# Kernel tuning notes

Measured on AMD Instinct MI355X. Metric: run time of the kernel, lower is better.

## Reference

```python
import jax, jax.numpy as jnp
import numpy as np

G = 3            # number of groups
K = 40           # per-group vector dim
CODEBOOK_SIZE = 1024
VQ_COMMIT = 0.25


def setup_inputs() -> dict:
    key = jax.random.key(0)
    k1, k2 = jax.random.split(key)
    z = jax.random.normal(k1, (32, 30, 16384), dtype=jnp.float32)
    codebooks = jax.random.normal(k2, (G, CODEBOOK_SIZE, K), dtype=jnp.float32)
    return {"z": z, "codebooks": codebooks}


def _group_vq(z, codebooks):
    N, C, T = z.shape
    # torch: z = reshape(z, (N, C*4, -1)); assert C*4 == K*G
    z4 = z.reshape(N, C * 4, T // 4)              # (N, G*K, T')
    Tp = z4.shape[2]
    # split channels into G contiguous blocks of K, flatten to vectors of dim K
    x = z4.reshape(N, G, K, Tp).transpose(1, 0, 3, 2).reshape(G, N * Tp, K)  # (G, M, K)
    # squared-L2 nearest-codeword search (cdist + argmin), batched over groups
    x2 = jnp.sum(x * x, axis=-1, keepdims=True)           # (G, M, 1)
    e2 = jnp.sum(codebooks * codebooks, axis=-1)          # (G, S)
    d = x2 + e2[:, None, :] - 2.0 * jnp.einsum('gmk,gsk->gms', x, codebooks)  # (G, M, S)
    idx = jnp.argmin(d, axis=-1)                          # (G, M)
    q = jax.vmap(lambda cb, i: cb[i])(codebooks, idx)     # (G, M, K)
    # torch loop overwrites vq_loss each iteration -> only last group's commitment loss survives
    vq_loss = VQ_COMMIT * jnp.mean((jax.lax.stop_gradient(q[-1]) - x[-1]) ** 2)
    # straight-through estimator
    q_st = x + jax.lax.stop_gradient(q - x)               # (G, M, K)
    # undo the group split/flatten, then reshape back to (N, C, T)
    q_merge = q_st.reshape(G, N, Tp, K).transpose(1, 0, 3, 2).reshape(N, G * K, Tp)
    q_merge = q_merge.reshape(N, C, T)
    return q_merge, vq_loss


def reference(z, codebooks):
    return _group_vq(z, codebooks)
```

## Files before the change

### kernel.cpp

```cpp
#include <hip/hip_runtime.h>

#define G 3
#define K 40
#define S 1024
#define NB 32
#define CH 30
#define T 16384
#define TP 4096
#define M 131072
#define CT (CH*T)
#define OUT_Q (NB*CH*T)
#define MARGIN 4e-3f
#define FLAGBIT 0x40000000u

typedef __attribute__((ext_vector_type(8))) short short8;
typedef __attribute__((ext_vector_type(4))) float f32x4;

#define WS_LOSS 0
#define WS_E2   64
#define WS_PX   12352

static __device__ __forceinline__ unsigned short f2bf(float f) {
    union { float f; unsigned int u; } v; v.f = f;
    unsigned int u = v.u;
    return (unsigned short)((u + 0x7fffu + ((u >> 16) & 1u)) >> 16);
}
static __device__ __forceinline__ float bf2f(unsigned short h) {
    union { unsigned int u; float f; } v; v.u = ((unsigned int)h) << 16;
    return v.f;
}


__global__ void vq_prep_frag(const float* __restrict__ cb, short8* __restrict__ PX,
                             float* __restrict__ e2, double* __restrict__ loss) {
    int t = blockIdx.x * 256 + threadIdx.x;
    if (t == 0) *loss = 0.0;
    if (t >= G * 64 * 64) return;
    const int lane = t & 63;
    const int st   = (t >> 6) & 63;
    const int g    = t >> 12;
    const int lmod = lane & 15, lgrp = lane >> 4;
    const int s0   = st * 16;
    const float* cbg = cb + (size_t)g * S * K;

    if (lane < 16) {
        const float* row = cbg + (size_t)(s0 + lane) * K;
        float acc = 0.f;
        #pragma unroll
        for (int k = 0; k < K; ++k) acc = fmaf(row[k], row[k], acc);
        e2[g * S + s0 + lane] = -0.5f * acc;
    }

    const float* crow = cbg + (size_t)(s0 + lmod) * K;
    #pragma unroll
    for (int m = 0; m < 4; ++m) {
        short8 P;
        #pragma unroll
        for (int j = 0; j < 8; ++j) {
            int kap = 32 * m + 8 * lgrp + j;
            bool valid = kap < 120;
            int d = (kap < 40) ? kap : ((kap < 80) ? kap - 40 : kap - 80);
            float v = valid ? crow[d] : 0.f;
            unsigned short hh = f2bf(v);
            unsigned short ll = f2bf(v - bf2f(hh));
            bool low = (kap >= 40) && (kap < 80);
            P[j] = (short)(low ? ll : hh);
        }
        PX[(((size_t)(g * 64 + st)) * 4 + m) * 64 + lane] = P;
    }
}

__global__ __launch_bounds__(256, 4) void vq_search(
        const float* __restrict__ z, const short8* __restrict__ PX,
        const float* __restrict__ e2, float* __restrict__ out) {
    __shared__ float sE2[S];

    const int lane = threadIdx.x & 63;
    const int w    = threadIdx.x >> 6;
    const int g    = blockIdx.x >> 10;
    const int qbase = ((blockIdx.x & 1023) << 7) + (w << 5);
    const int n    = qbase >> 12;
    const int tp0  = qbase & 4095;
    const int lmod = lane & 15, lgrp = lane >> 4;

    const float* zg  = z + (size_t)n * CT + (size_t)g * K * TP;
    const float* e2g = e2 + g * S;
    const short8* PXg = PX + ((size_t)g * 64) * 4 * 64;

    *(f32x4*)(sE2 + threadIdx.x * 4) = *(const f32x4*)(e2g + threadIdx.x * 4);

    short8 xq[2][4];
    #pragma unroll
    for (int mt = 0; mt < 2; ++mt) {
        int tp = tp0 + mt * 16 + lmod;
        #pragma unroll
        for (int m = 0; m < 4; ++m) {
            short8 xb;
            #pragma unroll
            for (int j = 0; j < 8; ++j) {
                int kap = 32 * m + 8 * lgrp + j;
                bool valid = kap < 120;
                int d = (kap < 40) ? kap : ((kap < 80) ? kap - 40 : kap - 80);
                float v = valid ? zg[(size_t)d * TP + tp] : 0.f;
                unsigned short hh = f2bf(v);
                unsigned short ll = f2bf(v - bf2f(hh));
                bool low = (kap >= 80) && (kap < 120);
                xb[j] = (short)(low ? ll : hh);
            }
            xq[mt][m] = xb;
        }
    }
    __syncthreads();

    float v1[2], v2[2]; int i1[2];
    #pragma unroll
    for (int mt = 0; mt < 2; ++mt) { v1[mt] = -3.4e38f; v2[mt] = -3.4e38f; i1[mt] = 0; }

#define COMPTILE(c0_, c1_, c2_, c3_, st_)                                               \
    do {                                                                                \
        f32x4 e2v = *(const f32x4*)(sE2 + (st_) * 16 + lgrp * 4);                       \
        const int sbase = (st_) * 16 + lgrp * 4;                                        \
        _Pragma("unroll")                                                               \
        for (int mt = 0; mt < 2; ++mt) {                                                \
            f32x4 d = __builtin_amdgcn_mfma_f32_16x16x32_bf16(c0_, xq[mt][0], e2v, 0, 0, 0); \
            d = __builtin_amdgcn_mfma_f32_16x16x32_bf16(c1_, xq[mt][1], d, 0, 0, 0);    \
            d = __builtin_amdgcn_mfma_f32_16x16x32_bf16(c2_, xq[mt][2], d, 0, 0, 0);    \
            d = __builtin_amdgcn_mfma_f32_16x16x32_bf16(c3_, xq[mt][3], d, 0, 0, 0);    \
            _Pragma("unroll")                                                           \
            for (int j = 0; j < 4; ++j) {                                               \
                float sj = d[j];                                                        \
                v2[mt] = __builtin_amdgcn_fmed3f(v1[mt], v2[mt], sj);                   \
                bool cc = sj > v1[mt];                                                  \
                v1[mt] = fmaxf(v1[mt], sj);                                             \
                i1[mt] = cc ? (sbase + j) : i1[mt];                                     \
            }                                                                           \
        }                                                                               \
    } while (0)

    short8 a0 = PXg[lane], a1 = PXg[64 + lane], a2 = PXg[128 + lane], a3 = PXg[192 + lane];
    short8 b0, b1, b2, b3;
    #pragma unroll 1
    for (int it = 0; it < 32; ++it) {
        const int st0 = 2 * it, st1 = 2 * it + 1;
        {
            const short8* pn = PXg + (size_t)st1 * 256 + lane;
            b0 = pn[0]; b1 = pn[64]; b2 = pn[128]; b3 = pn[192];
        }
        COMPTILE(a0, a1, a2, a3, st0);
        if (it < 31) {
            const short8* pn = PXg + (size_t)(st0 + 2) * 256 + lane;
            a0 = pn[0]; a1 = pn[64]; a2 = pn[128]; a3 = pn[192];
        }
        COMPTILE(b0, b1, b2, b3, st1);
    }
#undef COMPTILE

    int* slotbase = (int*)(out + (size_t)n * CT + (size_t)g * K * TP);
    #pragma unroll
    for (int mt = 0; mt < 2; ++mt) {
        float a1v = v1[mt], a2v = v2[mt];
        int ii = i1[mt];
        #pragma unroll
        for (int off = 16; off < 64; off <<= 1) {
            float p1 = __shfl_xor(a1v, off);
            float p2 = __shfl_xor(a2v, off);
            int   pi = __shfl_xor(ii, off);
            float lo = fminf(a1v, p1);
            a2v = fmaxf(fmaxf(a2v, p2), lo);
            bool take = (p1 > a1v) || (p1 == a1v && pi < ii);
            ii = take ? pi : ii;
            a1v = fmaxf(a1v, p1);
        }
        if (lane < 16) {
            unsigned int val = (unsigned int)ii | ((a1v - a2v < MARGIN) ? FLAGBIT : 0u);
            slotbase[tp0 + mt * 16 + lane] = (int)val;
        }
    }
}

__global__ __launch_bounds__(256, 2) void vq_fix(
        const float* __restrict__ z, const float* __restrict__ cb,
        float* __restrict__ out) {
    __shared__ float sXq[4][K];

    const int lane = threadIdx.x & 63;
    const int w    = threadIdx.x >> 6;
    const int gq0  = (blockIdx.x * 4 + w) * 64;
    const int g    = gq0 >> 17;
    const int mm   = gq0 & (M - 1);
    const int n    = mm >> 12;
    const int tp0  = mm & 4095;

    const float* zg  = z + (size_t)n * CT + (size_t)g * K * TP;
    const float* cbg = cb + (size_t)g * S * K;
    int* slotbase = (int*)(out + (size_t)n * CT + (size_t)g * K * TP);

    unsigned int val = (unsigned int)slotbase[tp0 + lane];
    unsigned long long mask = __ballot((val & FLAGBIT) != 0u);
    while (mask) {
        int qq = __ffsll((unsigned long long)mask) - 1; mask &= mask - 1;
        int tpq = tp0 + qq;
        __threadfence_block();
        if (lane < K) sXq[w][lane] = zg[(size_t)lane * TP + tpq];
        __threadfence_block();
        double bestv = 1e300; int besti = 0;
        #pragma unroll 2
        for (int si = 0; si < 16; ++si) {
            int s = lane * 16 + si;
            const f32x4* cr4 = (const f32x4*)(cbg + (size_t)s * K);
            f32x4 cv[10];
            #pragma unroll
            for (int i = 0; i < 10; ++i) cv[i] = cr4[i];
            double acc = 0.0, en = 0.0;
            #pragma unroll
            for (int i = 0; i < 10; ++i) {
                #pragma unroll
                for (int c = 0; c < 4; ++c) {
                    double ev = (double)cv[i][c];
                    acc = fma(ev, (double)sXq[w][i * 4 + c], acc);
                    en  = fma(ev, ev, en);
                }
            }
            double sc = 0.5 * en - acc;
            if (sc < bestv) { bestv = sc; besti = s; }
        }
        #pragma unroll
        for (int off = 1; off < 64; off <<= 1) {
            double pv = __shfl_xor(bestv, off);
            int    pi = __shfl_xor(besti, off);
            if (pv < bestv || (pv == bestv && pi < besti)) { bestv = pv; besti = pi; }
        }
        if (lane == 0) slotbase[tpq] = besti;
    }
}

__global__ __launch_bounds__(256) void vq_gather(
        const float* __restrict__ z, const float* __restrict__ cb,
        float* __restrict__ out, double* __restrict__ loss) {
    const int q0 = (blockIdx.x * 256 + threadIdx.x) * 4;
    const int g = q0 >> 17;
    const int m = q0 & (M - 1);
    const int n = m >> 12;
    const int tp = m & 4095;

    float* base = out + (size_t)n * CT + (size_t)g * K * TP;
    const int4 idx4 = *(const int4*)((const int*)base + tp);
    const float* cbg = cb + (size_t)g * S * K;
    const f32x4* c0 = (const f32x4*)(cbg + (size_t)(idx4.x & 1023) * K);
    const f32x4* c1 = (const f32x4*)(cbg + (size_t)(idx4.y & 1023) * K);
    const f32x4* c2 = (const f32x4*)(cbg + (size_t)(idx4.z & 1023) * K);
    const f32x4* c3 = (const f32x4*)(cbg + (size_t)(idx4.w & 1023) * K);
    const float* zr = z + (size_t)n * CT + (size_t)g * K * TP + tp;

    double lsum = 0.0;
    #pragma unroll
    for (int i = 0; i < 10; ++i) {
        f32x4 a = c0[i], b = c1[i], c = c2[i], d = c3[i];
        #pragma unroll
        for (int cc = 0; cc < 4; ++cc) {
            const int k = i * 4 + cc;
            f32x4 sv;
            sv[0] = a[cc]; sv[1] = b[cc]; sv[2] = c[cc]; sv[3] = d[cc];
            *(f32x4*)(base + (size_t)k * TP + tp) = sv;
            if (g == 2) {
                f32x4 xv = *(const f32x4*)(zr + (size_t)k * TP);
                #pragma unroll
                for (int j = 0; j < 4; ++j) {
                    double dd = (double)sv[j] - (double)xv[j];
                    lsum = fma(dd, dd, lsum);
                }
            }
        }
    }

    if (g == 2) {
        #pragma unroll
        for (int off = 1; off < 64; off <<= 1)
            lsum += __shfl_xor(lsum, off);
        if ((threadIdx.x & 63) == 0) atomicAdd(loss, lsum);
    }
}

__global__ void vq_fin_kernel(const double* __restrict__ loss, float* __restrict__ out) {
    out[OUT_Q] = (float)(0.25 * (*loss) / (double)((long long)M * K));
}

extern "C" void kernel_launch(void* const* d_in, const int* in_sizes, int n_in,
                              void* d_out, int out_size, void* d_ws, size_t ws_size,
                              hipStream_t stream) {
    const float* z  = (const float*)d_in[0];
    const float* cb = (const float*)d_in[1];
    float* out = (float*)d_out;

    char* ws = (char*)d_ws;
    double* loss = (double*)(ws + WS_LOSS);
    float*  e2   = (float*)(ws + WS_E2);
    short8* PX   = (short8*)(ws + WS_PX);

    vq_prep_frag<<<dim3(48), dim3(256), 0, stream>>>(cb, PX, e2, loss);
    vq_search<<<dim3(3072), dim3(256), 0, stream>>>(z, PX, e2, out);
    vq_fix<<<dim3((G * M) / 256), dim3(256), 0, stream>>>(z, cb, out);
    vq_gather<<<dim3((G * M) / 1024), dim3(256), 0, stream>>>(z, cb, out, loss);
    vq_fin_kernel<<<dim3(1), dim3(1), 0, stream>>>(loss, out);
}
```

Before: 216.2 us.

## Share codebook fragments via LDS double buffer and double rows per wave

Each wave now covers 64 query rows instead of 32, so every codebook fragment feeds four MFMA row tiles instead of two. Codebook fragments are no longer loaded by each wave from global memory. The four waves of a block now load them cooperatively into a double-buffered LDS tile, with a block barrier each iteration. Grid size halves and launch bounds drop to 3 blocks per CU to fit the larger register footprint, which trades occupancy and adds barrier cost in exchange for fewer global/L2 fragment loads.

```diff
diff --git a/kernel.cpp b/kernel.cpp
--- a/kernel.cpp
+++ b/kernel.cpp
@@ -70,28 +70,29 @@
     }
 }
 
-__global__ __launch_bounds__(256, 4) void vq_search(
+__global__ __launch_bounds__(256, 3) void vq_search(
         const float* __restrict__ z, const short8* __restrict__ PX,
         const float* __restrict__ e2, float* __restrict__ out) {
-    __shared__ float sE2[S];
+    __shared__ short8 frag[2][2][4][64];
+    __shared__ float  sE2[S];
 
     const int lane = threadIdx.x & 63;
     const int w    = threadIdx.x >> 6;
-    const int g    = blockIdx.x >> 10;
-    const int qbase = ((blockIdx.x & 1023) << 7) + (w << 5);
+    const int g    = blockIdx.x >> 9;
+    const int qbase = ((blockIdx.x & 511) << 8) + (w << 6);
     const int n    = qbase >> 12;
     const int tp0  = qbase & 4095;
     const int lmod = lane & 15, lgrp = lane >> 4;
 
     const float* zg  = z + (size_t)n * CT + (size_t)g * K * TP;
     const float* e2g = e2 + g * S;
-    const short8* PXg = PX + ((size_t)g * 64) * 4 * 64;
+    const short8* srcW = PX + ((size_t)g * 64) * 4 * 64 + w * 64 + lane;
 
     *(f32x4*)(sE2 + threadIdx.x * 4) = *(const f32x4*)(e2g + threadIdx.x * 4);
 
-    short8 xq[2][4];
-    #pragma unroll
-    for (int mt = 0; mt < 2; ++mt) {
+    short8 xq[4][4];
+    #pragma unroll
+    for (int mt = 0; mt < 4; ++mt) {
         int tp = tp0 + mt * 16 + lmod;
         #pragma unroll
         for (int m = 0; m < 4; ++m) {
@@ -110,54 +111,61 @@
             xq[mt][m] = xb;
         }
     }
+
+    float v1[4], v2[4]; int i1[4];
+    #pragma unroll
+    for (int mt = 0; mt < 4; ++mt) { v1[mt] = -3.4e38f; v2[mt] = -3.4e38f; i1[mt] = 0; }
+
+    frag[0][0][w][lane] = srcW[0];
+    frag[0][1][w][lane] = srcW[256];
     __syncthreads();
 
-    float v1[2], v2[2]; int i1[2];
-    #pragma unroll
-    for (int mt = 0; mt < 2; ++mt) { v1[mt] = -3.4e38f; v2[mt] = -3.4e38f; i1[mt] = 0; }
-
-#define COMPTILE(c0_, c1_, c2_, c3_, st_)                                               \
-    do {                                                                                \
-        f32x4 e2v = *(const f32x4*)(sE2 + (st_) * 16 + lgrp * 4);                       \
-        const int sbase = (st_) * 16 + lgrp * 4;                                        \
-        _Pragma("unroll")                                                               \
-        for (int mt = 0; mt < 2; ++mt) {                                                \
-            f32x4 d = __builtin_amdgcn_mfma_f32_16x16x32_bf16(c0_, xq[mt][0], e2v, 0, 0, 0); \
-            d = __builtin_amdgcn_mfma_f32_16x16x32_bf16(c1_, xq[mt][1], d, 0, 0, 0);    \
-            d = __builtin_amdgcn_mfma_f32_16x16x32_bf16(c2_, xq[mt][2], d, 0, 0, 0);    \
-            d = __builtin_amdgcn_mfma_f32_16x16x32_bf16(c3_, xq[mt][3], d, 0, 0, 0);    \
-            _Pragma("unroll")                                                           \
-            for (int j = 0; j < 4; ++j) {                                               \
-                float sj = d[j];                                                        \
-                v2[mt] = __builtin_amdgcn_fmed3f(v1[mt], v2[mt], sj);                   \
-                bool cc = sj > v1[mt];                                                  \
-                v1[mt] = fmaxf(v1[mt], sj);                                             \
-                i1[mt] = cc ? (sbase + j) : i1[mt];                                     \
-            }                                                                           \
-        }                                                                               \
-    } while (0)
-
-    short8 a0 = PXg[lane], a1 = PXg[64 + lane], a2 = PXg[128 + lane], a3 = PXg[192 + lane];
-    short8 b0, b1, b2, b3;
     #pragma unroll 1
     for (int it = 0; it < 32; ++it) {
-        const int st0 = 2 * it, st1 = 2 * it + 1;
-        {
-            const short8* pn = PXg + (size_t)st1 * 256 + lane;
-            b0 = pn[0]; b1 = pn[64]; b2 = pn[128]; b3 = pn[192];
-        }
-        COMPTILE(a0, a1, a2, a3, st0);
+        const int cbuf = it & 1, nbuf = cbuf ^ 1;
+        short8 nxtA, nxtB;
         if (it < 31) {
-            const short8* pn = PXg + (size_t)(st0 + 2) * 256 + lane;
-            a0 = pn[0]; a1 = pn[64]; a2 = pn[128]; a3 = pn[192];
-        }
-        COMPTILE(b0, b1, b2, b3, st1);
-    }
-#undef COMPTILE
+            nxtA = srcW[(size_t)(2 * it + 2) * 256];
+            nxtB = srcW[(size_t)(2 * it + 3) * 256];
+        }
+
+        #pragma unroll
+        for (int sub = 0; sub < 2; ++sub) {
+            const int st = 2 * it + sub;
+            short8 p0 = frag[cbuf][sub][0][lane];
+            short8 p1 = frag[cbuf][sub][1][lane];
+            short8 p2 = frag[cbuf][sub][2][lane];
+            short8 p3 = frag[cbuf][sub][3][lane];
+            f32x4 e2v = *(const f32x4*)(sE2 + st * 16 + lgrp * 4);
+            const int sbase = st * 16 + lgrp * 4;
+
+            #pragma unroll
+            for (int mt = 0; mt < 4; ++mt) {
+                f32x4 d = __builtin_amdgcn_mfma_f32_16x16x32_bf16(p0, xq[mt][0], e2v, 0, 0, 0);
+                d = __builtin_amdgcn_mfma_f32_16x16x32_bf16(p1, xq[mt][1], d, 0, 0, 0);
+                d = __builtin_amdgcn_mfma_f32_16x16x32_bf16(p2, xq[mt][2], d, 0, 0, 0);
+                d = __builtin_amdgcn_mfma_f32_16x16x32_bf16(p3, xq[mt][3], d, 0, 0, 0);
+                #pragma unroll
+                for (int j = 0; j < 4; ++j) {
+                    float sj = d[j];
+                    v2[mt] = __builtin_amdgcn_fmed3f(v1[mt], v2[mt], sj);
+                    bool cc = sj > v1[mt];
+                    v1[mt] = fmaxf(v1[mt], sj);
+                    i1[mt] = cc ? (sbase + j) : i1[mt];
+                }
+            }
+        }
+
+        if (it < 31) {
+            frag[nbuf][0][w][lane] = nxtA;
+            frag[nbuf][1][w][lane] = nxtB;
+        }
+        __syncthreads();
+    }
 
     int* slotbase = (int*)(out + (size_t)n * CT + (size_t)g * K * TP);
     #pragma unroll
-    for (int mt = 0; mt < 2; ++mt) {
+    for (int mt = 0; mt < 4; ++mt) {
         float a1v = v1[mt], a2v = v2[mt];
         int ii = i1[mt];
         #pragma unroll
@@ -298,7 +306,7 @@
     short8* PX   = (short8*)(ws + WS_PX);
 
     vq_prep_frag<<<dim3(48), dim3(256), 0, stream>>>(cb, PX, e2, loss);
-    vq_search<<<dim3(3072), dim3(256), 0, stream>>>(z, PX, e2, out);
+    vq_search<<<dim3(1536), dim3(256), 0, stream>>>(z, PX, e2, out);
     vq_fix<<<dim3((G * M) / 256), dim3(256), 0, stream>>>(z, cb, out);
     vq_gather<<<dim3((G * M) / 1024), dim3(256), 0, stream>>>(z, cb, out, loss);
     vq_fin_kernel<<<dim3(1), dim3(1), 0, stream>>>(loss, out);
```

Result: faster. 201.0 us (-7.0%).
